# Kernel tuning notes

Hardware: AMD Instinct MI355X
Metric: run time of the kernel (lower is better)

The kernel has to match this reference:

```python
import jax, jax.numpy as jnp
import numpy as np

B, M, K, C = 256, 512, 6, 32  # graphs, nodes/graph, knn k, channels
IN_DIM, OUT_DIM = 4, 6


def setup_inputs() -> dict:
    key = jax.random.key(0)
    ks = jax.random.split(key, 20)
    N = B * M
    x = jax.random.normal(ks[0], (N, 1), dtype=jnp.float32)
    pos = jax.random.uniform(ks[1], (N, 3), dtype=jnp.float32)
    batch = jnp.repeat(jnp.arange(B, dtype=jnp.int64), M)

    def lin(k, out_d, in_d):
        bound = 1.0 / np.sqrt(in_d)
        kw, kb = jax.random.split(k)
        W = jax.random.uniform(kw, (out_d, in_d), minval=-bound, maxval=bound, dtype=jnp.float32)
        b = jax.random.uniform(kb, (out_d,), minval=-bound, maxval=bound, dtype=jnp.float32)
        return W, b

    W1a, b1a = lin(ks[2], C, IN_DIM)
    W2a, b2a = lin(ks[3], C, C)
    W1b, b1b = lin(ks[4], C, C)
    W2b, b2b = lin(ks[5], C, C)
    W1c, b1c = lin(ks[6], C, C)
    W2c, b2c = lin(ks[7], C, C)
    Wr, br = lin(ks[8], OUT_DIM, C)
    return dict(x=x, pos=pos, batch=batch,
                W1a=W1a, b1a=b1a, W2a=W2a, b2a=b2a,
                W1b=W1b, b1b=b1b, W2b=W2b, b2b=b2b,
                W1c=W1c, b1c=b1c, W2c=W2c, b2c=b2c,
                Wr=Wr, br=br)


def knn_indices(pos3):
    # pos3: [B, M, 3] -> [B, M, K] indices of K nearest neighbors (self included, loop=True)
    sq = jnp.sum(pos3 * pos3, axis=-1)                      # [B, M]
    d2 = sq[:, :, None] + sq[:, None, :] - 2.0 * jnp.einsum('bmd,bnd->bmn', pos3, pos3)
    _, idx = jax.lax.top_k(-d2, K)                          # [B, M, K]
    return idx


def gcn_layer(h, idx, W1, b1, W2, b2):
    # h: [B, M, Cin]; gather h_j per edge, 2-layer MLP per edge, max-aggregate over neighbors
    Cin = h.shape[-1]
    nb = jnp.take_along_axis(h, idx.reshape(B, M * K, 1), axis=1).reshape(B, M, K, Cin)
    msg = jax.nn.relu(jnp.einsum('bmkc,oc->bmko', nb, W1) + b1)
    msg = jnp.einsum('bmkc,oc->bmko', msg, W2) + b2
    return jnp.max(msg, axis=2)                             # max aggregation -> [B, M, C]


def reference(x, pos, batch,
              W1a, b1a, W2a, b2a,
              W1b, b1b, W2b, b2b,
              W1c, b1c, W2c, b2c,
              Wr, br):
    pos3 = pos.reshape(B, M, 3)
    idx = knn_indices(pos3)
    h = jnp.concatenate([x, pos], axis=-1).reshape(B, M, IN_DIM)
    h = jax.nn.relu(gcn_layer(h, idx, W1a, b1a, W2a, b2a))
    h = jax.nn.relu(gcn_layer(h, idx, W1b, b1b, W2b, b2b))
    h = jax.nn.relu(gcn_layer(h, idx, W1c, b1c, W2c, b2c))
    g = jnp.max(h, axis=1)                                  # global_max_pool -> [B, C]
    return g @ Wr.T + br                                    # [B, 6]
```

## Files before the change

### kernel.cpp

```cpp
#include <hip/hip_runtime.h>
#include <cstddef>

#define NB 256
#define M 512
#define KNN 6
#define C 32
#define NTOT (NB*M)

__global__ __launch_bounds__(512) void knn_kernel(const float* __restrict__ pos,
                                                  int* __restrict__ idx)
{
    __shared__ float4 sp[M];
    __shared__ float  cd[512][7];
    __shared__ int    ci[512][7];

    const int b      = blockIdx.x;
    const int g      = b >> 2;
    const int rchunk = b & 3;
    const int tid    = threadIdx.x;

    const float* p = pos + (size_t)g * M * 3;
    for (int i = tid; i < M; i += 512) {
        float x = p[3 * i], y = p[3 * i + 1], z = p[3 * i + 2];
        sp[i] = make_float4(x, y, z, fmaf(x, x, fmaf(y, y, z * z)));
    }
    __syncthreads();

    const int part = tid >> 7;
    const int rloc = tid & 127;
    const int row  = rchunk * 128 + rloc;

    const float4 pm = sp[row];
    const float xm = pm.x, ym = pm.y, zm = pm.z, sqm = pm.w;

    float d[KNN]; int id[KNN];
#pragma unroll
    for (int k = 0; k < KNN; k++) { d[k] = INFINITY; id[k] = -1; }

    const int n0 = part * 128;
#pragma unroll 4
    for (int jj = 0; jj < 128; jj++) {
        const int n = n0 + jj;
        const float4 pn = sp[n];
        float dot  = fmaf(xm, pn.x, fmaf(ym, pn.y, zm * pn.z));
        float dist = fmaf(-2.f, dot, sqm + pn.w);
#pragma unroll
        for (int k = KNN - 1; k > 0; k--) {
            bool ck  = dist < d[k];
            bool ck1 = dist < d[k - 1];
            d[k]  = ck1 ? d[k - 1]  : (ck ? dist : d[k]);
            id[k] = ck1 ? id[k - 1] : (ck ? n    : id[k]);
        }
        bool c0 = dist < d[0];
        d[0]  = c0 ? dist : d[0];
        id[0] = c0 ? n    : id[0];
    }

#pragma unroll
    for (int k = 0; k < KNN; k++) { cd[tid][k] = d[k]; ci[tid][k] = id[k]; }
    __syncthreads();

    if (tid < 128) {
        float md[KNN]; int mi[KNN];
#pragma unroll
        for (int k = 0; k < KNN; k++) { md[k] = cd[tid][k]; mi[k] = ci[tid][k]; }
#pragma unroll
        for (int pp = 1; pp < 4; pp++) {
#pragma unroll
            for (int k = 0; k < KNN; k++) {
                float dist = cd[pp * 128 + tid][k];
                int   n    = ci[pp * 128 + tid][k];
#pragma unroll
                for (int q = KNN - 1; q > 0; q--) {
                    bool cq  = dist < md[q];
                    bool cq1 = dist < md[q - 1];
                    md[q] = cq1 ? md[q - 1] : (cq ? dist : md[q]);
                    mi[q] = cq1 ? mi[q - 1] : (cq ? n    : mi[q]);
                }
                bool c0 = dist < md[0];
                md[0] = c0 ? dist : md[0];
                mi[0] = c0 ? n    : mi[0];
            }
        }
        const int node = g * M + rchunk * 128 + tid;
#pragma unroll
        for (int k = 0; k < KNN; k++)
            idx[k * NTOT + node] = g * M + mi[k];
    }
}

template <int IN>
__device__ __forceinline__ void gcn_layer_fused(float (&h)[C],
    const float* __restrict__ W1, const float* __restrict__ b1,
    const float* __restrict__ W2, const float* __restrict__ b2,
    float* Ts, int t, const int (&j)[KNN])
{
    float m1[C];
#pragma unroll
    for (int o = 0; o < C; o++) {
        float a = b1[o];
#pragma unroll
        for (int i = 0; i < IN; i++) a = fmaf(W1[o * IN + i], h[i], a);
        m1[o] = fmaxf(a, 0.f);
    }

    const int tp = t & 7;
#pragma unroll
    for (int q = 0; q < 8; q++) {
        float4 v;
        float* vp = &v.x;
#pragma unroll
        for (int u = 0; u < 4; u++) {
            const int o = 4 * q + u;
            float a = b2[o];
#pragma unroll
            for (int i = 0; i < C; i++) a = fmaf(W2[o * C + i], m1[i], a);
            vp[u] = a;
        }
        *(float4*)&Ts[t * C + ((q ^ tp) << 2)] = v;
    }
    __syncthreads();

#pragma unroll
    for (int c = 0; c < C; c++) h[c] = -INFINITY;
#pragma unroll
    for (int k = 0; k < KNN; k++) {
        const int jl = j[k], jp = jl & 7;
#pragma unroll
        for (int q = 0; q < 8; q++) {
            const float4 v = *(const float4*)&Ts[jl * C + ((q ^ jp) << 2)];
            h[4*q+0] = fmaxf(h[4*q+0], v.x);
            h[4*q+1] = fmaxf(h[4*q+1], v.y);
            h[4*q+2] = fmaxf(h[4*q+2], v.z);
            h[4*q+3] = fmaxf(h[4*q+3], v.w);
        }
    }
#pragma unroll
    for (int c = 0; c < C; c++) h[c] = fmaxf(h[c], 0.f);
    __syncthreads();
}

__global__ __launch_bounds__(512, 1) void fused_kernel(
    const float* __restrict__ x, const float* __restrict__ pos,
    const int* __restrict__ idx,
    const float* __restrict__ W1a, const float* __restrict__ b1a,
    const float* __restrict__ W2a, const float* __restrict__ b2a,
    const float* __restrict__ W1b, const float* __restrict__ b1b,
    const float* __restrict__ W2b, const float* __restrict__ b2b,
    const float* __restrict__ W1c, const float* __restrict__ b1c,
    const float* __restrict__ W2c, const float* __restrict__ b2c,
    const float* __restrict__ Wr,  const float* __restrict__ br,
    float* __restrict__ out)
{
    __shared__ __align__(16) float Ts[M * C];
    const int g = blockIdx.x, t = threadIdx.x;
    const int n = g * M + t;

    int j[KNN];
#pragma unroll
    for (int k = 0; k < KNN; k++) j[k] = idx[k * NTOT + n] & (M - 1);

    float h[C];
    h[0] = x[n];
    h[1] = pos[3 * n];
    h[2] = pos[3 * n + 1];
    h[3] = pos[3 * n + 2];

    gcn_layer_fused<4>(h, W1a, b1a, W2a, b2a, Ts, t, j);
    gcn_layer_fused<C>(h, W1b, b1b, W2b, b2b, Ts, t, j);
    gcn_layer_fused<C>(h, W1c, b1c, W2c, b2c, Ts, t, j);

    const int tp = t & 7;
#pragma unroll
    for (int q = 0; q < 8; q++) {
        float4 v = make_float4(h[4*q], h[4*q+1], h[4*q+2], h[4*q+3]);
        *(float4*)&Ts[t * C + ((q ^ tp) << 2)] = v;
    }
    __syncthreads();

    for (int s = 256; s >= 32; s >>= 1) {
        if (t < s) {
#pragma unroll
            for (int q = 0; q < 8; q++) {
                const int ph = (q ^ tp) << 2;
                float4 a = *(const float4*)&Ts[t * C + ph];
                float4 b = *(const float4*)&Ts[(t + s) * C + ph];
                a.x = fmaxf(a.x, b.x); a.y = fmaxf(a.y, b.y);
                a.z = fmaxf(a.z, b.z); a.w = fmaxf(a.w, b.w);
                *(float4*)&Ts[t * C + ph] = a;
            }
        }
        __syncthreads();
    }

    if (t < C) {
        float m = -INFINITY;
#pragma unroll
        for (int r = 0; r < 32; r++)
            m = fmaxf(m, Ts[r * C + ((((t >> 2) ^ (r & 7)) << 2) | (t & 3))]);
        Ts[t] = m;
    }
    __syncthreads();

    if (t < 6) {
        float a = br[t];
#pragma unroll
        for (int i = 0; i < C; i++) a = fmaf(Wr[t * C + i], Ts[i], a);
        out[g * 6 + t] = a;
    }
}

extern "C" void kernel_launch(void* const* d_in, const int* in_sizes, int n_in,
                              void* d_out, int out_size, void* d_ws, size_t ws_size,
                              hipStream_t stream) {
    const float* x   = (const float*)d_in[0];
    const float* pos = (const float*)d_in[1];
    const float* W1a = (const float*)d_in[3];
    const float* b1a = (const float*)d_in[4];
    const float* W2a = (const float*)d_in[5];
    const float* b2a = (const float*)d_in[6];
    const float* W1b = (const float*)d_in[7];
    const float* b1b = (const float*)d_in[8];
    const float* W2b = (const float*)d_in[9];
    const float* b2b = (const float*)d_in[10];
    const float* W1c = (const float*)d_in[11];
    const float* b1c = (const float*)d_in[12];
    const float* W2c = (const float*)d_in[13];
    const float* b2c = (const float*)d_in[14];
    const float* Wr  = (const float*)d_in[15];
    const float* br  = (const float*)d_in[16];

    int*   idx = (int*)d_ws;
    float* out = (float*)d_out;

    knn_kernel<<<NB * 4, 512, 0, stream>>>(pos, idx);

    fused_kernel<<<NB, 512, 0, stream>>>(x, pos, idx,
                                         W1a, b1a, W2a, b2a,
                                         W1b, b1b, W2b, b2b,
                                         W1c, b1c, W2c, b2c,
                                         Wr, br, out);
}
```

Measured before the change: 203.3 us.

## Process two query rows per thread in knn kernel, halving blocks

Each knn thread now computes distances for two query rows against its candidate slice, so every shared-memory load of a candidate point is reused twice, and the grid shrinks from 4 to 2 blocks per graph. The merge buffers double in size, with indices stored as unsigned short to limit shared-memory growth, and 256 threads perform the final merge. The cost is more registers per thread and fewer blocks in flight, which may lower occupancy and latency hiding.

Result: no change. 204.6 us (+0.6%).

```diff
diff --git a/kernel.cpp b/kernel.cpp
--- a/kernel.cpp
+++ b/kernel.cpp
@@ -11,13 +11,13 @@
                                                   int* __restrict__ idx)
 {
     __shared__ float4 sp[M];
-    __shared__ float  cd[512][7];
-    __shared__ int    ci[512][7];
-
-    const int b      = blockIdx.x;
-    const int g      = b >> 2;
-    const int rchunk = b & 3;
-    const int tid    = threadIdx.x;
+    __shared__ float  cd[1024][7];
+    __shared__ unsigned short ci[1024][7];
+
+    const int b    = blockIdx.x;
+    const int g    = b >> 1;
+    const int half = b & 1;
+    const int tid  = threadIdx.x;
 
     const float* p = pos + (size_t)g * M * 3;
     for (int i = tid; i < M; i += 512) {
@@ -28,48 +28,76 @@
 
     const int part = tid >> 7;
     const int rloc = tid & 127;
-    const int row  = rchunk * 128 + rloc;
-
-    const float4 pm = sp[row];
-    const float xm = pm.x, ym = pm.y, zm = pm.z, sqm = pm.w;
-
-    float d[KNN]; int id[KNN];
-#pragma unroll
-    for (int k = 0; k < KNN; k++) { d[k] = INFINITY; id[k] = -1; }
+    const int ra   = half * 256 + rloc;
+    const int rb   = ra + 128;
+
+    const float4 pa = sp[ra];
+    const float4 pb = sp[rb];
+
+    float da[KNN], db[KNN];
+    int   ia[KNN], ib[KNN];
+#pragma unroll
+    for (int k = 0; k < KNN; k++) {
+        da[k] = INFINITY; db[k] = INFINITY; ia[k] = -1; ib[k] = -1;
+    }
 
     const int n0 = part * 128;
 #pragma unroll 4
     for (int jj = 0; jj < 128; jj++) {
         const int n = n0 + jj;
         const float4 pn = sp[n];
-        float dot  = fmaf(xm, pn.x, fmaf(ym, pn.y, zm * pn.z));
-        float dist = fmaf(-2.f, dot, sqm + pn.w);
+
+        float dotA = fmaf(pa.x, pn.x, fmaf(pa.y, pn.y, pa.z * pn.z));
+        float dA   = fmaf(-2.f, dotA, pa.w + pn.w);
+        float dotB = fmaf(pb.x, pn.x, fmaf(pb.y, pn.y, pb.z * pn.z));
+        float dB   = fmaf(-2.f, dotB, pb.w + pn.w);
+
 #pragma unroll
         for (int k = KNN - 1; k > 0; k--) {
-            bool ck  = dist < d[k];
-            bool ck1 = dist < d[k - 1];
-            d[k]  = ck1 ? d[k - 1]  : (ck ? dist : d[k]);
-            id[k] = ck1 ? id[k - 1] : (ck ? n    : id[k]);
-        }
-        bool c0 = dist < d[0];
-        d[0]  = c0 ? dist : d[0];
-        id[0] = c0 ? n    : id[0];
-    }
-
-#pragma unroll
-    for (int k = 0; k < KNN; k++) { cd[tid][k] = d[k]; ci[tid][k] = id[k]; }
-    __syncthreads();
-
-    if (tid < 128) {
+            bool ck  = dA < da[k];
+            bool ck1 = dA < da[k - 1];
+            da[k] = ck1 ? da[k - 1] : (ck ? dA : da[k]);
+            ia[k] = ck1 ? ia[k - 1] : (ck ? n  : ia[k]);
+        }
+        bool cA = dA < da[0];
+        da[0] = cA ? dA : da[0];
+        ia[0] = cA ? n  : ia[0];
+
+#pragma unroll
+        for (int k = KNN - 1; k > 0; k--) {
+            bool ck  = dB < db[k];
+            bool ck1 = dB < db[k - 1];
+            db[k] = ck1 ? db[k - 1] : (ck ? dB : db[k]);
+            ib[k] = ck1 ? ib[k - 1] : (ck ? n  : ib[k]);
+        }
+        bool cB = dB < db[0];
+        db[0] = cB ? dB : db[0];
+        ib[0] = cB ? n  : ib[0];
+    }
+
+    {
+        const int La = part * 256 + rloc;
+        const int Lb = La + 128;
+#pragma unroll
+        for (int k = 0; k < KNN; k++) {
+            cd[La][k] = da[k]; ci[La][k] = (unsigned short)ia[k];
+            cd[Lb][k] = db[k]; ci[Lb][k] = (unsigned short)ib[k];
+        }
+    }
+    __syncthreads();
+
+    if (tid < 256) {
+        const int m = tid;
         float md[KNN]; int mi[KNN];
 #pragma unroll
-        for (int k = 0; k < KNN; k++) { md[k] = cd[tid][k]; mi[k] = ci[tid][k]; }
+        for (int k = 0; k < KNN; k++) { md[k] = cd[m][k]; mi[k] = ci[m][k]; }
 #pragma unroll
         for (int pp = 1; pp < 4; pp++) {
+            const int L = pp * 256 + m;
 #pragma unroll
             for (int k = 0; k < KNN; k++) {
-                float dist = cd[pp * 128 + tid][k];
-                int   n    = ci[pp * 128 + tid][k];
+                float dist = cd[L][k];
+                int   n    = ci[L][k];
 #pragma unroll
                 for (int q = KNN - 1; q > 0; q--) {
                     bool cq  = dist < md[q];
@@ -82,7 +110,7 @@
                 mi[0] = c0 ? n    : mi[0];
             }
         }
-        const int node = g * M + rchunk * 128 + tid;
+        const int node = g * M + half * 256 + m;
 #pragma unroll
         for (int k = 0; k < KNN; k++)
             idx[k * NTOT + node] = g * M + mi[k];
@@ -233,7 +261,7 @@
     int*   idx = (int*)d_ws;
     float* out = (float*)d_out;
 
-    knn_kernel<<<NB * 4, 512, 0, stream>>>(pos, idx);
+    knn_kernel<<<NB * 2, 512, 0, stream>>>(pos, idx);
 
     fused_kernel<<<NB, 512, 0, stream>>>(x, pos, idx,
                                          W1a, b1a, W2a, b2a,
```

## Fuse kNN and GCN layers into one 1024-thread kernel per graph

Applied to the files above, without the earlier changes.

Merges the kNN kernel and the GCN kernel into a single kernel with one 1024-thread block per graph. Each node is handled by two threads: each scans half the candidate columns for kNN, and each computes half of the W2 output channels. Neighbour indices stay in shared memory as 16-bit values, which removes the global round trip of idx and the second launch. In exchange, the grid drops from 1024 kNN blocks to 256 blocks. Each thread still computes the full W1 layer, so that work is duplicated, and the extra syncthreads lengthen the serial chain within each block.

Result: no change. 202.1 us (-0.6%).

```diff
diff --git a/kernel.cpp b/kernel.cpp
--- a/kernel.cpp
+++ b/kernel.cpp
@@ -5,144 +5,9 @@
 #define M 512
 #define KNN 6
 #define C 32
-#define NTOT (NB*M)
-
-__global__ __launch_bounds__(512) void knn_kernel(const float* __restrict__ pos,
-                                                  int* __restrict__ idx)
-{
-    __shared__ float4 sp[M];
-    __shared__ float  cd[512][7];
-    __shared__ int    ci[512][7];
-
-    const int b      = blockIdx.x;
-    const int g      = b >> 2;
-    const int rchunk = b & 3;
-    const int tid    = threadIdx.x;
-
-    const float* p = pos + (size_t)g * M * 3;
-    for (int i = tid; i < M; i += 512) {
-        float x = p[3 * i], y = p[3 * i + 1], z = p[3 * i + 2];
-        sp[i] = make_float4(x, y, z, fmaf(x, x, fmaf(y, y, z * z)));
-    }
-    __syncthreads();
-
-    const int part = tid >> 7;
-    const int rloc = tid & 127;
-    const int row  = rchunk * 128 + rloc;
-
-    const float4 pm = sp[row];
-    const float xm = pm.x, ym = pm.y, zm = pm.z, sqm = pm.w;
-
-    float d[KNN]; int id[KNN];
-#pragma unroll
-    for (int k = 0; k < KNN; k++) { d[k] = INFINITY; id[k] = -1; }
-
-    const int n0 = part * 128;
-#pragma unroll 4
-    for (int jj = 0; jj < 128; jj++) {
-        const int n = n0 + jj;
-        const float4 pn = sp[n];
-        float dot  = fmaf(xm, pn.x, fmaf(ym, pn.y, zm * pn.z));
-        float dist = fmaf(-2.f, dot, sqm + pn.w);
-#pragma unroll
-        for (int k = KNN - 1; k > 0; k--) {
-            bool ck  = dist < d[k];
-            bool ck1 = dist < d[k - 1];
-            d[k]  = ck1 ? d[k - 1]  : (ck ? dist : d[k]);
-            id[k] = ck1 ? id[k - 1] : (ck ? n    : id[k]);
-        }
-        bool c0 = dist < d[0];
-        d[0]  = c0 ? dist : d[0];
-        id[0] = c0 ? n    : id[0];
-    }
-
-#pragma unroll
-    for (int k = 0; k < KNN; k++) { cd[tid][k] = d[k]; ci[tid][k] = id[k]; }
-    __syncthreads();
-
-    if (tid < 128) {
-        float md[KNN]; int mi[KNN];
-#pragma unroll
-        for (int k = 0; k < KNN; k++) { md[k] = cd[tid][k]; mi[k] = ci[tid][k]; }
-#pragma unroll
-        for (int pp = 1; pp < 4; pp++) {
-#pragma unroll
-            for (int k = 0; k < KNN; k++) {
-                float dist = cd[pp * 128 + tid][k];
-                int   n    = ci[pp * 128 + tid][k];
-#pragma unroll
-                for (int q = KNN - 1; q > 0; q--) {
-                    bool cq  = dist < md[q];
-                    bool cq1 = dist < md[q - 1];
-                    md[q] = cq1 ? md[q - 1] : (cq ? dist : md[q]);
-                    mi[q] = cq1 ? mi[q - 1] : (cq ? n    : mi[q]);
-                }
-                bool c0 = dist < md[0];
-                md[0] = c0 ? dist : md[0];
-                mi[0] = c0 ? n    : mi[0];
-            }
-        }
-        const int node = g * M + rchunk * 128 + tid;
-#pragma unroll
-        for (int k = 0; k < KNN; k++)
-            idx[k * NTOT + node] = g * M + mi[k];
-    }
-}
-
-template <int IN>
-__device__ __forceinline__ void gcn_layer_fused(float (&h)[C],
-    const float* __restrict__ W1, const float* __restrict__ b1,
-    const float* __restrict__ W2, const float* __restrict__ b2,
-    float* Ts, int t, const int (&j)[KNN])
-{
-    float m1[C];
-#pragma unroll
-    for (int o = 0; o < C; o++) {
-        float a = b1[o];
-#pragma unroll
-        for (int i = 0; i < IN; i++) a = fmaf(W1[o * IN + i], h[i], a);
-        m1[o] = fmaxf(a, 0.f);
-    }
-
-    const int tp = t & 7;
-#pragma unroll
-    for (int q = 0; q < 8; q++) {
-        float4 v;
-        float* vp = &v.x;
-#pragma unroll
-        for (int u = 0; u < 4; u++) {
-            const int o = 4 * q + u;
-            float a = b2[o];
-#pragma unroll
-            for (int i = 0; i < C; i++) a = fmaf(W2[o * C + i], m1[i], a);
-            vp[u] = a;
-        }
-        *(float4*)&Ts[t * C + ((q ^ tp) << 2)] = v;
-    }
-    __syncthreads();
-
-#pragma unroll
-    for (int c = 0; c < C; c++) h[c] = -INFINITY;
-#pragma unroll
-    for (int k = 0; k < KNN; k++) {
-        const int jl = j[k], jp = jl & 7;
-#pragma unroll
-        for (int q = 0; q < 8; q++) {
-            const float4 v = *(const float4*)&Ts[jl * C + ((q ^ jp) << 2)];
-            h[4*q+0] = fmaxf(h[4*q+0], v.x);
-            h[4*q+1] = fmaxf(h[4*q+1], v.y);
-            h[4*q+2] = fmaxf(h[4*q+2], v.z);
-            h[4*q+3] = fmaxf(h[4*q+3], v.w);
-        }
-    }
-#pragma unroll
-    for (int c = 0; c < C; c++) h[c] = fmaxf(h[c], 0.f);
-    __syncthreads();
-}
-
-__global__ __launch_bounds__(512, 1) void fused_kernel(
+
+__global__ __launch_bounds__(1024, 1) void megafused_kernel(
     const float* __restrict__ x, const float* __restrict__ pos,
-    const int* __restrict__ idx,
     const float* __restrict__ W1a, const float* __restrict__ b1a,
     const float* __restrict__ W2a, const float* __restrict__ b2a,
     const float* __restrict__ W1b, const float* __restrict__ b1b,
@@ -153,41 +18,216 @@
     float* __restrict__ out)
 {
     __shared__ __align__(16) float Ts[M * C];
-    const int g = blockIdx.x, t = threadIdx.x;
-    const int n = g * M + t;
+    const int g  = blockIdx.x;
+    const int t  = threadIdx.x;
+    const int n  = t & (M - 1);
+    const int hv = t >> 9;
+    const int c0 = __builtin_amdgcn_readfirstlane(hv << 4);
+
+    float4* sp          = (float4*)Ts;
+    float*  cd          = Ts + 2048;
+    unsigned short* ci  = (unsigned short*)(Ts + 2048 + 7168);
+
+    const float* p = pos + (size_t)g * M * 3;
+    if (t < M) {
+        float xx = p[3*t], yy = p[3*t+1], zz = p[3*t+2];
+        sp[t] = make_float4(xx, yy, zz, fmaf(xx, xx, fmaf(yy, yy, zz * zz)));
+    }
+    __syncthreads();
+
+    const float4 pm = sp[n];
+
+    float d[KNN]; int id[KNN];
+#pragma unroll
+    for (int k = 0; k < KNN; k++) { d[k] = INFINITY; id[k] = -1; }
+
+    const int col0 = hv << 8;
+#pragma unroll 4
+    for (int jj = 0; jj < 256; jj++) {
+        const int col = col0 + jj;
+        const float4 pn = sp[col];
+        float dot  = fmaf(pm.x, pn.x, fmaf(pm.y, pn.y, pm.z * pn.z));
+        float dist = fmaf(-2.f, dot, pm.w + pn.w);
+#pragma unroll
+        for (int k = KNN - 1; k > 0; k--) {
+            bool ck  = dist < d[k];
+            bool ck1 = dist < d[k - 1];
+            d[k]  = ck1 ? d[k - 1]  : (ck ? dist : d[k]);
+            id[k] = ck1 ? id[k - 1] : (ck ? col  : id[k]);
+        }
+        bool c0b = dist < d[0];
+        d[0]  = c0b ? dist : d[0];
+        id[0] = c0b ? col  : id[0];
+    }
+#pragma unroll
+    for (int k = 0; k < KNN; k++) {
+        cd[t * 7 + k] = d[k];
+        ci[t * 7 + k] = (unsigned short)id[k];
+    }
+    __syncthreads();
 
     int j[KNN];
-#pragma unroll
-    for (int k = 0; k < KNN; k++) j[k] = idx[k * NTOT + n] & (M - 1);
-
-    float h[C];
-    h[0] = x[n];
-    h[1] = pos[3 * n];
-    h[2] = pos[3 * n + 1];
-    h[3] = pos[3 * n + 2];
-
-    gcn_layer_fused<4>(h, W1a, b1a, W2a, b2a, Ts, t, j);
-    gcn_layer_fused<C>(h, W1b, b1b, W2b, b2b, Ts, t, j);
-    gcn_layer_fused<C>(h, W1c, b1c, W2c, b2c, Ts, t, j);
+    {
+        float md[KNN]; int mi[KNN];
+#pragma unroll
+        for (int k = 0; k < KNN; k++) { md[k] = cd[n*7 + k]; mi[k] = ci[n*7 + k]; }
+        const int L1 = (n + M) * 7;
+#pragma unroll
+        for (int k = 0; k < KNN; k++) {
+            float dist = cd[L1 + k];
+            int   nn   = ci[L1 + k];
+#pragma unroll
+            for (int q = KNN - 1; q > 0; q--) {
+                bool cq  = dist < md[q];
+                bool cq1 = dist < md[q - 1];
+                md[q] = cq1 ? md[q - 1] : (cq ? dist : md[q]);
+                mi[q] = cq1 ? mi[q - 1] : (cq ? nn   : mi[q]);
+            }
+            bool cb = dist < md[0];
+            md[0] = cb ? dist : md[0];
+            mi[0] = cb ? nn   : mi[0];
+        }
+#pragma unroll
+        for (int k = 0; k < KNN; k++) j[k] = mi[k];
+    }
+    __syncthreads();
+
+    const int np = n & 7;
+
+    {
+        const float h0 = x[(size_t)g * M + n];
+        const float h1 = pm.x, h2 = pm.y, h3 = pm.z;
+        float m1[C];
+#pragma unroll
+        for (int o = 0; o < C; o++) {
+            float a = b1a[o];
+            a = fmaf(W1a[o*4+0], h0, a);
+            a = fmaf(W1a[o*4+1], h1, a);
+            a = fmaf(W1a[o*4+2], h2, a);
+            a = fmaf(W1a[o*4+3], h3, a);
+            m1[o] = fmaxf(a, 0.f);
+        }
+#pragma unroll
+        for (int q2 = 0; q2 < 4; q2++) {
+            float4 v; float* vp = &v.x;
+#pragma unroll
+            for (int u = 0; u < 4; u++) {
+                const int o = c0 + q2*4 + u;
+                float a = b2a[o];
+#pragma unroll
+                for (int i = 0; i < C; i++) a = fmaf(W2a[o*C + i], m1[i], a);
+                vp[u] = a;
+            }
+            const int q = 4*hv + q2;
+            *(float4*)&Ts[n*C + ((q ^ np) << 2)] = v;
+        }
+    }
+    __syncthreads();
+
+#pragma unroll 1
+    for (int layer = 0; layer < 2; layer++) {
+        const float* W1 = layer ? W1c : W1b;
+        const float* b1 = layer ? b1c : b1b;
+        const float* W2 = layer ? W2c : W2b;
+        const float* b2 = layer ? b2c : b2b;
+
+        float hm[16];
+#pragma unroll
+        for (int u = 0; u < 16; u++) hm[u] = -INFINITY;
+#pragma unroll
+        for (int k = 0; k < KNN; k++) {
+            const int jl = j[k], jp = jl & 7;
+#pragma unroll
+            for (int q2 = 0; q2 < 4; q2++) {
+                const int q = 4*hv + q2;
+                const float4 v = *(const float4*)&Ts[jl*C + ((q ^ jp) << 2)];
+                hm[4*q2+0] = fmaxf(hm[4*q2+0], v.x);
+                hm[4*q2+1] = fmaxf(hm[4*q2+1], v.y);
+                hm[4*q2+2] = fmaxf(hm[4*q2+2], v.z);
+                hm[4*q2+3] = fmaxf(hm[4*q2+3], v.w);
+            }
+        }
+#pragma unroll
+        for (int u = 0; u < 16; u++) hm[u] = fmaxf(hm[u], 0.f);
+        __syncthreads();
+#pragma unroll
+        for (int q2 = 0; q2 < 4; q2++) {
+            const int q = 4*hv + q2;
+            *(float4*)&Ts[n*C + ((q ^ np) << 2)] =
+                make_float4(hm[4*q2], hm[4*q2+1], hm[4*q2+2], hm[4*q2+3]);
+        }
+        __syncthreads();
+        float hf[C];
+#pragma unroll
+        for (int q = 0; q < 8; q++) {
+            const float4 v = *(const float4*)&Ts[n*C + ((q ^ np) << 2)];
+            hf[4*q+0] = v.x; hf[4*q+1] = v.y; hf[4*q+2] = v.z; hf[4*q+3] = v.w;
+        }
+        __syncthreads();
+        float m1[C];
+#pragma unroll
+        for (int o = 0; o < C; o++) {
+            float a = b1[o];
+#pragma unroll
+            for (int i = 0; i < C; i++) a = fmaf(W1[o*C + i], hf[i], a);
+            m1[o] = fmaxf(a, 0.f);
+        }
+#pragma unroll
+        for (int q2 = 0; q2 < 4; q2++) {
+            float4 v; float* vp = &v.x;
+#pragma unroll
+            for (int u = 0; u < 4; u++) {
+                const int o = c0 + q2*4 + u;
+                float a = b2[o];
+#pragma unroll
+                for (int i = 0; i < C; i++) a = fmaf(W2[o*C + i], m1[i], a);
+                vp[u] = a;
+            }
+            const int q = 4*hv + q2;
+            *(float4*)&Ts[n*C + ((q ^ np) << 2)] = v;
+        }
+        __syncthreads();
+    }
+
+    {
+        float hm[16];
+#pragma unroll
+        for (int u = 0; u < 16; u++) hm[u] = -INFINITY;
+#pragma unroll
+        for (int k = 0; k < KNN; k++) {
+            const int jl = j[k], jp = jl & 7;
+#pragma unroll
+            for (int q2 = 0; q2 < 4; q2++) {
+                const int q = 4*hv + q2;
+                const float4 v = *(const float4*)&Ts[jl*C + ((q ^ jp) << 2)];
+                hm[4*q2+0] = fmaxf(hm[4*q2+0], v.x);
+                hm[4*q2+1] = fmaxf(hm[4*q2+1], v.y);
+                hm[4*q2+2] = fmaxf(hm[4*q2+2], v.z);
+                hm[4*q2+3] = fmaxf(hm[4*q2+3], v.w);
+            }
+        }
+        __syncthreads();
+#pragma unroll
+        for (int q2 = 0; q2 < 4; q2++) {
+            const int q = 4*hv + q2;
+            *(float4*)&Ts[n*C + ((q ^ np) << 2)] =
+                make_float4(fmaxf(hm[4*q2+0], 0.f), fmaxf(hm[4*q2+1], 0.f),
+                            fmaxf(hm[4*q2+2], 0.f), fmaxf(hm[4*q2+3], 0.f));
+        }
+        __syncthreads();
+    }
 
     const int tp = t & 7;
-#pragma unroll
-    for (int q = 0; q < 8; q++) {
-        float4 v = make_float4(h[4*q], h[4*q+1], h[4*q+2], h[4*q+3]);
-        *(float4*)&Ts[t * C + ((q ^ tp) << 2)] = v;
-    }
-    __syncthreads();
-
     for (int s = 256; s >= 32; s >>= 1) {
         if (t < s) {
 #pragma unroll
             for (int q = 0; q < 8; q++) {
                 const int ph = (q ^ tp) << 2;
-                float4 a = *(const float4*)&Ts[t * C + ph];
-                float4 b = *(const float4*)&Ts[(t + s) * C + ph];
+                float4 a = *(const float4*)&Ts[t*C + ph];
+                float4 b = *(const float4*)&Ts[(t + s)*C + ph];
                 a.x = fmaxf(a.x, b.x); a.y = fmaxf(a.y, b.y);
                 a.z = fmaxf(a.z, b.z); a.w = fmaxf(a.w, b.w);
-                *(float4*)&Ts[t * C + ph] = a;
+                *(float4*)&Ts[t*C + ph] = a;
             }
         }
         __syncthreads();
@@ -197,7 +237,7 @@
         float m = -INFINITY;
 #pragma unroll
         for (int r = 0; r < 32; r++)
-            m = fmaxf(m, Ts[r * C + ((((t >> 2) ^ (r & 7)) << 2) | (t & 3))]);
+            m = fmaxf(m, Ts[r*C + ((((t >> 2) ^ (r & 7)) << 2) | (t & 3))]);
         Ts[t] = m;
     }
     __syncthreads();
@@ -205,7 +245,7 @@
     if (t < 6) {
         float a = br[t];
 #pragma unroll
-        for (int i = 0; i < C; i++) a = fmaf(Wr[t * C + i], Ts[i], a);
+        for (int i = 0; i < C; i++) a = fmaf(Wr[t*C + i], Ts[i], a);
         out[g * 6 + t] = a;
     }
 }
@@ -230,14 +270,11 @@
     const float* Wr  = (const float*)d_in[15];
     const float* br  = (const float*)d_in[16];
 
-    int*   idx = (int*)d_ws;
     float* out = (float*)d_out;
 
-    knn_kernel<<<NB * 4, 512, 0, stream>>>(pos, idx);
-
-    fused_kernel<<<NB, 512, 0, stream>>>(x, pos, idx,
-                                         W1a, b1a, W2a, b2a,
-                                         W1b, b1b, W2b, b2b,
-                                         W1c, b1c, W2c, b2c,
-                                         Wr, br, out);
+    megafused_kernel<<<NB, 1024, 0, stream>>>(x, pos,
+                                              W1a, b1a, W2a, b2a,
+                                              W1b, b1b, W2b, b2b,
+                                              W1c, b1c, W2c, b2c,
+                                              Wr, br, out);
 }
```
